# Performance work log

Measured on AMD Instinct MI355X. Metric: run time of the kernel, lower is better.

## Reference

```python
import jax, jax.numpy as jnp
import numpy as np

B, S, H = 64, 2048, 512
VOCAB = 40000


def setup_inputs() -> dict:
    key = jax.random.key(0)
    k1, k2, k3, k4, k5 = jax.random.split(key, 5)
    token_ids = jax.random.randint(k1, (B, S), 0, VOCAB, dtype=jnp.int64) if jax.config.jax_enable_x64 else jax.random.randint(k1, (B, S), 0, VOCAB, dtype=jnp.int32)
    std = 0.02
    pos_table = jax.random.normal(k2, (S, H), dtype=jnp.float32) * std
    nest_table = jax.random.normal(k3, (16, H), dtype=jnp.float32) * std
    seg_table = jax.random.normal(k4, (8, H), dtype=jnp.float32) * std
    W = jax.random.normal(k5, (3 * H, H), dtype=jnp.float32) * (1.0 / np.sqrt(3 * H))
    return {"token_ids": token_ids, "pos_table": pos_table, "nest_table": nest_table, "seg_table": seg_table, "W": W}


def _syntax_info(token_ids):
    # Parallel replacement for the serial per-token loop.
    t = token_ids
    opens = (t == 40) | (t == 123) | (t == 91)
    closes = (t == 41) | (t == 125) | (t == 93)
    delta = opens.astype(jnp.int32) - closes.astype(jnp.int32)
    s = jnp.cumsum(delta, axis=1)  # unclamped walk
    # Lindley recursion level_i = max(0, level_{i-1} + d_i)
    #   == s_i - min(0, min_{j<=i} s_j)
    run_min = jax.lax.cummin(s, axis=1)
    nesting = jnp.clip(s - jnp.minimum(run_min, 0), 0, 15)
    segments = jnp.cumsum((t > 39990).astype(jnp.int32), axis=1) % 8
    return nesting, segments


def reference(token_ids, pos_table, nest_table, seg_table, W):
    b, s = token_ids.shape
    positions = jnp.arange(s)
    pos_emb = jnp.broadcast_to(pos_table[positions][None], (b, s, pos_table.shape[-1]))
    nesting, segments = _syntax_info(token_ids)
    nest_emb = nest_table[nesting]      # [B,S,H]
    seg_emb = seg_table[segments]       # [B,S,H]
    combined = jnp.concatenate([pos_emb, nest_emb, seg_emb], axis=-1)  # [B,S,3H]
    return jnp.einsum('bsk,kh->bsh', combined, W)
```

## Files before the change

### kernel.cpp

```cpp
#include <hip/hip_runtime.h>
#include <cstdint>

#define BB 64
#define SS 2048
#define HH 512

__global__ __launch_bounds__(256) void scan_kernel(const int* __restrict__ tok,
                                                   int* __restrict__ idx) {
    const int b = blockIdx.x;
    const int tid = threadIdx.x;
    const int* t = tok + (size_t)b * SS;

    int4 w0 = reinterpret_cast<const int4*>(t)[tid * 2 + 0];
    int4 w1 = reinterpret_cast<const int4*>(t)[tid * 2 + 1];
    int tk[8] = {w0.x, w0.y, w0.z, w0.w, w1.x, w1.y, w1.z, w1.w};

    int ls[8], lmin[8], lseg[8];
    int s = 0, m = 2147483647, sg = 0;
#pragma unroll
    for (int j = 0; j < 8; ++j) {
        int v = tk[j];
        int open_ = (v == 40) | (v == 123) | (v == 91);
        int close_ = (v == 41) | (v == 125) | (v == 93);
        s += open_ - close_;
        m = min(m, s);
        sg += (v > 39990) ? 1 : 0;
        ls[j] = s; lmin[j] = m; lseg[j] = sg;
    }

    __shared__ int sS[256], sM[256], sG[256];
    sS[tid] = s; sM[tid] = m; sG[tid] = sg;
    __syncthreads();
    for (int off = 1; off < 256; off <<= 1) {
        int aS = 0, aM = 2147483647, aG = 0;
        bool has = (tid >= off);
        if (has) { aS = sS[tid - off]; aM = sM[tid - off]; aG = sG[tid - off]; }
        __syncthreads();
        if (has) {
            sM[tid] = min(aM, aS + sM[tid]);
            sS[tid] = aS + sS[tid];
            sG[tid] = aG + sG[tid];
        }
        __syncthreads();
    }
    int pS = 0, pM = 2147483647, pG = 0;
    if (tid > 0) { pS = sS[tid - 1]; pM = sM[tid - 1]; pG = sG[tid - 1]; }

    int res[8];
#pragma unroll
    for (int j = 0; j < 8; ++j) {
        int gs = pS + ls[j];
        int rm = min(pM, pS + lmin[j]);
        int nest = gs - min(rm, 0);
        nest = max(0, min(15, nest));
        int seg = (pG + lseg[j]) & 7;
        res[j] = nest * 8 + seg;
    }
    int4* op = reinterpret_cast<int4*>(idx + (size_t)b * SS + tid * 8);
    op[0] = make_int4(res[0], res[1], res[2], res[3]);
    op[1] = make_int4(res[4], res[5], res[6], res[7]);
}

__global__ __launch_bounds__(256) void gemm_kernel(const float* __restrict__ A,
                                                   const float* __restrict__ Wm,
                                                   float* __restrict__ C, int M) {
    __shared__ float As[16][64];
    __shared__ float Bs[16][64];
    const int bm = blockIdx.x * 64;
    const int bn = blockIdx.y * 64;
    const int tid = threadIdx.x;
    const int tx = tid & 15;
    const int ty = tid >> 4;

    float acc[4][4];
#pragma unroll
    for (int i = 0; i < 4; ++i)
#pragma unroll
        for (int j = 0; j < 4; ++j) acc[i][j] = 0.0f;

    for (int k0 = 0; k0 < 512; k0 += 16) {
        {
            int mm = tid >> 2;
            int kq = (tid & 3) << 2;
            float4 av = make_float4(0.f, 0.f, 0.f, 0.f);
            int gm = bm + mm;
            if (gm < M)
                av = *reinterpret_cast<const float4*>(A + (size_t)gm * 512 + k0 + kq);
            As[kq + 0][mm] = av.x; As[kq + 1][mm] = av.y;
            As[kq + 2][mm] = av.z; As[kq + 3][mm] = av.w;
        }
        {
            int kk = tid >> 4;
            int nn = (tid & 15) << 2;
            float4 bv = *reinterpret_cast<const float4*>(
                Wm + (size_t)(k0 + kk) * 512 + bn + nn);
            *reinterpret_cast<float4*>(&Bs[kk][nn]) = bv;
        }
        __syncthreads();
#pragma unroll
        for (int kk = 0; kk < 16; ++kk) {
            float4 a = *reinterpret_cast<const float4*>(&As[kk][ty << 2]);
            float4 b = *reinterpret_cast<const float4*>(&Bs[kk][tx << 2]);
            float av_[4] = {a.x, a.y, a.z, a.w};
            float bv_[4] = {b.x, b.y, b.z, b.w};
#pragma unroll
            for (int i = 0; i < 4; ++i)
#pragma unroll
                for (int j = 0; j < 4; ++j) acc[i][j] += av_[i] * bv_[j];
        }
        __syncthreads();
    }
#pragma unroll
    for (int i = 0; i < 4; ++i) {
        int row = bm + (ty << 2) + i;
        if (row < M) {
            float4 o = make_float4(acc[i][0], acc[i][1], acc[i][2], acc[i][3]);
            *reinterpret_cast<float4*>(C + (size_t)row * 512 + bn + (tx << 2)) = o;
        }
    }
}

__global__ __launch_bounds__(256) void out_kernel(const float4* __restrict__ P,
                                                  const float4* __restrict__ N,
                                                  const float4* __restrict__ G,
                                                  const int* __restrict__ idx,
                                                  float4* __restrict__ out) {
    const int blk = blockIdx.x;
    const int s = blk >> 5;
    const int bp = blk & 31;
    const int ty = threadIdx.x >> 7;
    const int tx = threadIdx.x & 127;
    const int b = bp * 2 + ty;
    const size_t r = (size_t)b * SS + s;

    const int id = idx[r];
    const int n = id >> 3;
    const int g = id & 7;

    float4 p = P[(size_t)s * 128 + tx];
    float4 nv = N[(size_t)n * 128 + tx];
    float4 gv = G[(size_t)g * 128 + tx];
    float4 o;
    o.x = p.x + nv.x + gv.x;
    o.y = p.y + nv.y + gv.y;
    o.z = p.z + nv.z + gv.z;
    o.w = p.w + nv.w + gv.w;
    out[r * 128 + tx] = o;
}

extern "C" void kernel_launch(void* const* d_in, const int* in_sizes, int n_in,
                              void* d_out, int out_size, void* d_ws, size_t ws_size,
                              hipStream_t stream) {
    const int* tok = (const int*)d_in[0];
    const float* pos = (const float*)d_in[1];
    const float* nest = (const float*)d_in[2];
    const float* seg = (const float*)d_in[3];
    const float* W = (const float*)d_in[4];
    float* out = (float*)d_out;

    char* ws = (char*)d_ws;
    int* idx = (int*)ws;
    float* P = (float*)(ws + 524288);
    float* N = (float*)(ws + 524288 + 4194304);
    float* G = (float*)(ws + 524288 + 4194304 + 32768);

    scan_kernel<<<BB, 256, 0, stream>>>(tok, idx);
    gemm_kernel<<<dim3(32, 8), 256, 0, stream>>>(pos, W, P, 2048);
    gemm_kernel<<<dim3(1, 8), 256, 0, stream>>>(nest, W + 512 * 512, N, 16);
    gemm_kernel<<<dim3(1, 8), 256, 0, stream>>>(seg, W + 1024 * 512, G, 8);
    out_kernel<<<SS * 32, 256, 0, stream>>>(
        (const float4*)P, (const float4*)N, (const float4*)G, idx, (float4*)out);
}
```

Baseline: 386.2 us.

## Fuse scan and small GEMMs into one prep kernel, batch rows per output block

Merges the token scan, the position-table GEMM and the nest/segment table projections into a single kernel launch that dispatches on block index. The GEMM gains register prefetch of the next tile and a padded shared-memory layout, and the tiny table projections become simple per-column dot products. The output kernel now handles four batch rows per thread and reuses the loaded position vector across them. This cuts launch overhead and per-block setup, but the output stage stays bound by writing the 256 MiB result.

```diff
diff --git a/kernel.cpp b/kernel.cpp
--- a/kernel.cpp
+++ b/kernel.cpp
@@ -3,149 +3,150 @@
 
 #define BB 64
 #define SS 2048
-#define HH 512
 
-__global__ __launch_bounds__(256) void scan_kernel(const int* __restrict__ tok,
-                                                   int* __restrict__ idx) {
-    const int b = blockIdx.x;
+__global__ __launch_bounds__(256) void prep_kernel(
+    const int* __restrict__ tok, const float* __restrict__ pos,
+    const float* __restrict__ nest, const float* __restrict__ seg,
+    const float* __restrict__ W,
+    int* __restrict__ idx, float* __restrict__ P, float* __restrict__ NG) {
+    const int blk = blockIdx.x;
     const int tid = threadIdx.x;
-    const int* t = tok + (size_t)b * SS;
 
-    int4 w0 = reinterpret_cast<const int4*>(t)[tid * 2 + 0];
-    int4 w1 = reinterpret_cast<const int4*>(t)[tid * 2 + 1];
-    int tk[8] = {w0.x, w0.y, w0.z, w0.w, w1.x, w1.y, w1.z, w1.w};
+    if (blk < 256) {
+        __shared__ float As[16][68];
+        __shared__ float Bs[16][64];
+        const int bm = (blk >> 3) << 6;
+        const int bn = (blk & 7) << 6;
+        const int am = tid >> 2, ak = (tid & 3) << 2;
+        const int bk = tid >> 4, bn2 = (tid & 15) << 2;
+        const int tn = tid & 15, tm = tid >> 4;
 
-    int ls[8], lmin[8], lseg[8];
-    int s = 0, m = 2147483647, sg = 0;
+        const float* Ap = pos + (size_t)(bm + am) * 512 + ak;
+        const float* Bp = W + (size_t)bk * 512 + bn + bn2;
+        float4 aR = *(const float4*)Ap;
+        float4 bR = *(const float4*)Bp;
+
+        float acc[4][4];
 #pragma unroll
-    for (int j = 0; j < 8; ++j) {
-        int v = tk[j];
-        int open_ = (v == 40) | (v == 123) | (v == 91);
-        int close_ = (v == 41) | (v == 125) | (v == 93);
-        s += open_ - close_;
-        m = min(m, s);
-        sg += (v > 39990) ? 1 : 0;
-        ls[j] = s; lmin[j] = m; lseg[j] = sg;
-    }
+        for (int i = 0; i < 4; ++i)
+#pragma unroll
+            for (int j = 0; j < 4; ++j) acc[i][j] = 0.0f;
 
-    __shared__ int sS[256], sM[256], sG[256];
-    sS[tid] = s; sM[tid] = m; sG[tid] = sg;
-    __syncthreads();
-    for (int off = 1; off < 256; off <<= 1) {
-        int aS = 0, aM = 2147483647, aG = 0;
-        bool has = (tid >= off);
-        if (has) { aS = sS[tid - off]; aM = sM[tid - off]; aG = sG[tid - off]; }
+        for (int k0 = 0; k0 < 512; k0 += 16) {
+            __syncthreads();
+            As[ak + 0][am] = aR.x; As[ak + 1][am] = aR.y;
+            As[ak + 2][am] = aR.z; As[ak + 3][am] = aR.w;
+            *(float4*)&Bs[bk][bn2] = bR;
+            __syncthreads();
+            if (k0 + 16 < 512) {
+                aR = *(const float4*)(Ap + k0 + 16);
+                bR = *(const float4*)(Bp + (size_t)(k0 + 16) * 512);
+            }
+#pragma unroll
+            for (int kk = 0; kk < 16; ++kk) {
+                float4 a = *(const float4*)&As[kk][tm << 2];
+                float4 b = *(const float4*)&Bs[kk][tn << 2];
+                float av[4] = {a.x, a.y, a.z, a.w};
+                float bv[4] = {b.x, b.y, b.z, b.w};
+#pragma unroll
+                for (int i = 0; i < 4; ++i)
+#pragma unroll
+                    for (int j = 0; j < 4; ++j) acc[i][j] += av[i] * bv[j];
+            }
+        }
+#pragma unroll
+        for (int i = 0; i < 4; ++i) {
+            float4 o = make_float4(acc[i][0], acc[i][1], acc[i][2], acc[i][3]);
+            *(float4*)(P + (size_t)(bm + (tm << 2) + i) * 512 + bn + (tn << 2)) = o;
+        }
+    } else if (blk < 304) {
+        const int b2 = blk - 256;
+        const int row = b2 >> 1;
+        const int col = ((b2 & 1) << 8) + tid;
+        const float* Ta = (row < 16) ? (nest + (size_t)row * 512)
+                                     : (seg + (size_t)(row - 16) * 512);
+        const float* Wx = W + ((row < 16) ? (size_t)512 * 512 : (size_t)1024 * 512);
+        float s = 0.0f;
+#pragma unroll 8
+        for (int k = 0; k < 512; ++k) s += Ta[k] * Wx[(size_t)k * 512 + col];
+        NG[(size_t)row * 512 + col] = s;
+    } else {
+        __shared__ int sS[256], sM[256], sG[256];
+        const int b = blk - 304;
+        const int* t = tok + (size_t)b * SS;
+        int4 w0 = reinterpret_cast<const int4*>(t)[tid * 2 + 0];
+        int4 w1 = reinterpret_cast<const int4*>(t)[tid * 2 + 1];
+        int tk[8] = {w0.x, w0.y, w0.z, w0.w, w1.x, w1.y, w1.z, w1.w};
+
+        int ls[8], lmin[8], lseg[8];
+        int s = 0, m = 2147483647, sg = 0;
+#pragma unroll
+        for (int j = 0; j < 8; ++j) {
+            int v = tk[j];
+            int open_ = (v == 40) | (v == 123) | (v == 91);
+            int close_ = (v == 41) | (v == 125) | (v == 93);
+            s += open_ - close_;
+            m = min(m, s);
+            sg += (v > 39990) ? 1 : 0;
+            ls[j] = s; lmin[j] = m; lseg[j] = sg;
+        }
+        sS[tid] = s; sM[tid] = m; sG[tid] = sg;
         __syncthreads();
-        if (has) {
-            sM[tid] = min(aM, aS + sM[tid]);
-            sS[tid] = aS + sS[tid];
-            sG[tid] = aG + sG[tid];
+        for (int off = 1; off < 256; off <<= 1) {
+            int aS = 0, aM = 2147483647, aG = 0;
+            bool has = (tid >= off);
+            if (has) { aS = sS[tid - off]; aM = sM[tid - off]; aG = sG[tid - off]; }
+            __syncthreads();
+            if (has) {
+                sM[tid] = min(aM, aS + sM[tid]);
+                sS[tid] = aS + sS[tid];
+                sG[tid] = aG + sG[tid];
+            }
+            __syncthreads();
         }
-        __syncthreads();
-    }
-    int pS = 0, pM = 2147483647, pG = 0;
-    if (tid > 0) { pS = sS[tid - 1]; pM = sM[tid - 1]; pG = sG[tid - 1]; }
+        int pS = 0, pM = 2147483647, pG = 0;
+        if (tid > 0) { pS = sS[tid - 1]; pM = sM[tid - 1]; pG = sG[tid - 1]; }
 
-    int res[8];
+        int res[8];
 #pragma unroll
-    for (int j = 0; j < 8; ++j) {
-        int gs = pS + ls[j];
-        int rm = min(pM, pS + lmin[j]);
-        int nest = gs - min(rm, 0);
-        nest = max(0, min(15, nest));
-        int seg = (pG + lseg[j]) & 7;
-        res[j] = nest * 8 + seg;
-    }
-    int4* op = reinterpret_cast<int4*>(idx + (size_t)b * SS + tid * 8);
-    op[0] = make_int4(res[0], res[1], res[2], res[3]);
-    op[1] = make_int4(res[4], res[5], res[6], res[7]);
-}
-
-__global__ __launch_bounds__(256) void gemm_kernel(const float* __restrict__ A,
-                                                   const float* __restrict__ Wm,
-                                                   float* __restrict__ C, int M) {
-    __shared__ float As[16][64];
-    __shared__ float Bs[16][64];
-    const int bm = blockIdx.x * 64;
-    const int bn = blockIdx.y * 64;
-    const int tid = threadIdx.x;
-    const int tx = tid & 15;
-    const int ty = tid >> 4;
-
-    float acc[4][4];
-#pragma unroll
-    for (int i = 0; i < 4; ++i)
-#pragma unroll
-        for (int j = 0; j < 4; ++j) acc[i][j] = 0.0f;
-
-    for (int k0 = 0; k0 < 512; k0 += 16) {
-        {
-            int mm = tid >> 2;
-            int kq = (tid & 3) << 2;
-            float4 av = make_float4(0.f, 0.f, 0.f, 0.f);
-            int gm = bm + mm;
-            if (gm < M)
-                av = *reinterpret_cast<const float4*>(A + (size_t)gm * 512 + k0 + kq);
-            As[kq + 0][mm] = av.x; As[kq + 1][mm] = av.y;
-            As[kq + 2][mm] = av.z; As[kq + 3][mm] = av.w;
+        for (int j = 0; j < 8; ++j) {
+            int gs = pS + ls[j];
+            int rm = min(pM, pS + lmin[j]);
+            int nst = gs - min(rm, 0);
+            nst = max(0, min(15, nst));
+            int sgm = (pG + lseg[j]) & 7;
+            res[j] = nst * 8 + sgm;
         }
-        {
-            int kk = tid >> 4;
-            int nn = (tid & 15) << 2;
-            float4 bv = *reinterpret_cast<const float4*>(
-                Wm + (size_t)(k0 + kk) * 512 + bn + nn);
-            *reinterpret_cast<float4*>(&Bs[kk][nn]) = bv;
-        }
-        __syncthreads();
-#pragma unroll
-        for (int kk = 0; kk < 16; ++kk) {
-            float4 a = *reinterpret_cast<const float4*>(&As[kk][ty << 2]);
-            float4 b = *reinterpret_cast<const float4*>(&Bs[kk][tx << 2]);
-            float av_[4] = {a.x, a.y, a.z, a.w};
-            float bv_[4] = {b.x, b.y, b.z, b.w};
-#pragma unroll
-            for (int i = 0; i < 4; ++i)
-#pragma unroll
-                for (int j = 0; j < 4; ++j) acc[i][j] += av_[i] * bv_[j];
-        }
-        __syncthreads();
-    }
-#pragma unroll
-    for (int i = 0; i < 4; ++i) {
-        int row = bm + (ty << 2) + i;
-        if (row < M) {
-            float4 o = make_float4(acc[i][0], acc[i][1], acc[i][2], acc[i][3]);
-            *reinterpret_cast<float4*>(C + (size_t)row * 512 + bn + (tx << 2)) = o;
-        }
+        int4* op = reinterpret_cast<int4*>(idx + (size_t)b * SS + tid * 8);
+        op[0] = make_int4(res[0], res[1], res[2], res[3]);
+        op[1] = make_int4(res[4], res[5], res[6], res[7]);
     }
 }
 
 __global__ __launch_bounds__(256) void out_kernel(const float4* __restrict__ P,
-                                                  const float4* __restrict__ N,
-                                                  const float4* __restrict__ G,
+                                                  const float4* __restrict__ NG,
                                                   const int* __restrict__ idx,
                                                   float4* __restrict__ out) {
-    const int blk = blockIdx.x;
-    const int s = blk >> 5;
-    const int bp = blk & 31;
-    const int ty = threadIdx.x >> 7;
+    const int s = blockIdx.x >> 3;
+    const int bg = blockIdx.x & 7;
     const int tx = threadIdx.x & 127;
-    const int b = bp * 2 + ty;
-    const size_t r = (size_t)b * SS + s;
+    const int tz = threadIdx.x >> 7;
 
-    const int id = idx[r];
-    const int n = id >> 3;
-    const int g = id & 7;
-
-    float4 p = P[(size_t)s * 128 + tx];
-    float4 nv = N[(size_t)n * 128 + tx];
-    float4 gv = G[(size_t)g * 128 + tx];
-    float4 o;
-    o.x = p.x + nv.x + gv.x;
-    o.y = p.y + nv.y + gv.y;
-    o.z = p.z + nv.z + gv.z;
-    o.w = p.w + nv.w + gv.w;
-    out[r * 128 + tx] = o;
+    const float4 p = P[(size_t)s * 128 + tx];
+#pragma unroll
+    for (int i = 0; i < 4; ++i) {
+        const int b = (bg << 3) + (i << 1) + tz;
+        const size_t r = (size_t)b * SS + s;
+        const int id = idx[r];
+        const float4 nv = NG[(size_t)(id >> 3) * 128 + tx];
+        const float4 gv = NG[(size_t)(16 + (id & 7)) * 128 + tx];
+        float4 o;
+        o.x = p.x + nv.x + gv.x;
+        o.y = p.y + nv.y + gv.y;
+        o.z = p.z + nv.z + gv.z;
+        o.w = p.w + nv.w + gv.w;
+        out[r * 128 + tx] = o;
+    }
 }
 
 extern "C" void kernel_launch(void* const* d_in, const int* in_sizes, int n_in,
@@ -160,14 +161,10 @@
 
     char* ws = (char*)d_ws;
     int* idx = (int*)ws;
-    float* P = (float*)(ws + 524288);
-    float* N = (float*)(ws + 524288 + 4194304);
-    float* G = (float*)(ws + 524288 + 4194304 + 32768);
+    float* P = (float*)(ws + (512 << 10));
+    float* NG = (float*)(ws + (512 << 10) + (4 << 20));
 
-    scan_kernel<<<BB, 256, 0, stream>>>(tok, idx);
-    gemm_kernel<<<dim3(32, 8), 256, 0, stream>>>(pos, W, P, 2048);
-    gemm_kernel<<<dim3(1, 8), 256, 0, stream>>>(nest, W + 512 * 512, N, 16);
-    gemm_kernel<<<dim3(1, 8), 256, 0, stream>>>(seg, W + 1024 * 512, G, 8);
-    out_kernel<<<SS * 32, 256, 0, stream>>>(
-        (const float4*)P, (const float4*)N, (const float4*)G, idx, (float4*)out);
+    prep_kernel<<<368, 256, 0, stream>>>(tok, pos, nest, seg, W, idx, P, NG);
+    out_kernel<<<SS * 8, 256, 0, stream>>>(
+        (const float4*)P, (const float4*)NG, idx, (float4*)out);
 }
```

After: 310.8 us. 19.5% less time.
